# Performance work log

Hardware: AMD Instinct MI355X
Metric: run time of the kernel (lower is better)

## Reference

```python
import jax, jax.numpy as jnp
import numpy as np

# Module hyperparameters (from init_kwargs)
DG = 8          # deformable_groups
KH = KW = 3     # kernel size
STRIDE = 1
PAD = 1
DIL = 1


def conv2d(x, w, b):
    # x: [B,C,H,W], w: [O,I,kh,kw] -> [B,O,Ho,Wo]
    y = jax.lax.conv_general_dilated(
        x, w, window_strides=(STRIDE, STRIDE),
        padding=[(PAD, PAD), (PAD, PAD)],
        rhs_dilation=(DIL, DIL),
        dimension_numbers=('NCHW', 'OIHW', 'NCHW'))
    return y + b[None, :, None, None]


def deform_conv2d(inp, offset, mask, w, b):
    # torchvision.ops.DeformConv2d (v2, with modulation mask), groups=1.
    # offset: [B, 2*DG*K, Ho, Wo] laid out as (dg, k, (dy,dx));
    # mask:   [B, DG*K, Ho, Wo] (already sigmoided).
    B, C, H, W = inp.shape
    Cout = w.shape[0]
    K = KH * KW
    Ho, Wo = offset.shape[2], offset.shape[3]
    Cg = C // DG

    off = offset.reshape(B, DG, K, 2, Ho, Wo)
    # base sampling grid per kernel tap
    ky = jnp.repeat(jnp.arange(KH) * DIL, KW)        # [K]
    kx = jnp.tile(jnp.arange(KW) * DIL, KH)          # [K]
    ybase = jnp.arange(Ho) * STRIDE - PAD            # [Ho]
    xbase = jnp.arange(Wo) * STRIDE - PAD            # [Wo]
    ys = off[:, :, :, 0] + (ky[:, None, None] + ybase[None, :, None])  # [B,DG,K,Ho,Wo]
    xs = off[:, :, :, 1] + (kx[:, None, None] + xbase[None, None, :])

    y0 = jnp.floor(ys)
    x0 = jnp.floor(xs)
    wy = (ys - y0)[:, :, None]   # [B,DG,1,K,Ho,Wo]
    wx = (xs - x0)[:, :, None]
    y0i = y0.astype(jnp.int32)
    x0i = x0.astype(jnp.int32)

    flat = inp.reshape(B, DG, Cg, H * W)

    def gather(yi, xi):
        valid = (yi >= 0) & (yi < H) & (xi >= 0) & (xi < W)        # [B,DG,K,Ho,Wo]
        idx = jnp.clip(yi, 0, H - 1) * W + jnp.clip(xi, 0, W - 1)
        idxf = idx.reshape(B, DG, -1)
        g = jax.vmap(jax.vmap(lambda f, i: jnp.take(f, i, axis=1)))(flat, idxf)
        g = g.reshape(B, DG, Cg, K, Ho, Wo)
        return g * valid[:, :, None].astype(inp.dtype)

    v00 = gather(y0i, x0i)
    v01 = gather(y0i, x0i + 1)
    v10 = gather(y0i + 1, x0i)
    v11 = gather(y0i + 1, x0i + 1)
    val = (v00 * (1 - wy) * (1 - wx) + v01 * (1 - wy) * wx
           + v10 * wy * (1 - wx) + v11 * wy * wx)
    val = val * mask.reshape(B, DG, 1, K, Ho, Wo)
    val = val.reshape(B, C, K, Ho, Wo)
    out = jnp.einsum('bckhw,ock->bohw', val, w.reshape(Cout, C, K))
    return out + b[None, :, None, None]


def setup_inputs() -> dict:
    key = jax.random.key(0)
    ks = jax.random.split(key, 8)
    B, C, Cf, Cout, H, W = 4, 64, 64, 64, 128, 128
    K = KH * KW
    inp = jax.random.normal(ks[0], (B, C, H, W), jnp.float32)
    feature = jax.random.normal(ks[1], (B, Cf, H, W), jnp.float32)
    # conv_offset / conv_mask params (small init so sampled offsets stay local)
    w_off = 0.05 * jax.random.normal(ks[2], (2 * DG * K, Cf, KH, KW), jnp.float32)
    b_off = jnp.zeros((2 * DG * K,), jnp.float32)
    w_mask = 0.05 * jax.random.normal(ks[3], (DG * K, Cf, KH, KW), jnp.float32)
    b_mask = jnp.zeros((DG * K,), jnp.float32)
    # deform conv params
    fan_in = C * KH * KW
    w_dcn = jax.random.normal(ks[4], (Cout, C, KH, KW), jnp.float32) / np.sqrt(fan_in)
    b_dcn = 0.01 * jax.random.normal(ks[5], (Cout,), jnp.float32)
    return {"input": inp, "feature": feature,
            "w_off": w_off, "b_off": b_off,
            "w_mask": w_mask, "b_mask": b_mask,
            "w_dcn": w_dcn, "b_dcn": b_dcn}


def reference(input, feature, w_off, b_off, w_mask, b_mask, w_dcn, b_dcn):
    offset = conv2d(feature, w_off, b_off)
    mask = jax.nn.sigmoid(conv2d(feature, w_mask, b_mask))
    return deform_conv2d(input, offset, mask, w_dcn, b_dcn)
```

## Files before the change

### kernel.cpp

```cpp
#include <hip/hip_runtime.h>
#include <hip/hip_bf16.h>

#define NB 4
#define CIN 64
#define COUT 64
#define HH 128
#define WW 128
#define HW (HH*WW)
#define C_OFF 144
#define C_OM 216
#define C_PAD 224
#define KTOT 576

typedef __attribute__((ext_vector_type(8))) short bf16x8;
typedef __attribute__((ext_vector_type(4))) float f32x4;
typedef __attribute__((ext_vector_type(8))) unsigned short uv8;

__device__ inline unsigned short f2bf(float f) {
    union { float f; unsigned u; } v; v.f = f;
    unsigned r = (v.u + 0x7FFF + ((v.u >> 16) & 1)) >> 16;
    return (unsigned short)r;
}

__device__ inline float bf2f(unsigned short h) {
    union { unsigned u; float f; } v; v.u = ((unsigned)h) << 16; return v.f;
}


__global__ __launch_bounds__(256) void transpose_wdcn(const float* __restrict__ w,
                                                      float* __restrict__ wT) {
    int idx = blockIdx.x * 256 + threadIdx.x;
    if (idx < KTOT * COUT) {
        int o = idx & 63, kk = idx >> 6;
        wT[idx] = w[o * KTOT + kk];
    }
}

__global__ __launch_bounds__(256) void to_nhwc_bf16(const float* __restrict__ f,
                                                    unsigned short* __restrict__ o) {
    int t = blockIdx.x * 256 + threadIdx.x;
    int b = t >> 14, yx = t & 16383;
    const float* src = f + (size_t)b * CIN * HW + yx;
    unsigned short* dst = o + (size_t)t * 64;
#pragma unroll
    for (int c8 = 0; c8 < 8; ++c8) {
        uv8 v;
#pragma unroll
        for (int j = 0; j < 8; ++j) v[j] = f2bf(src[(size_t)(c8 * 8 + j) * HW]);
        *(uv8*)(dst + c8 * 8) = v;
    }
}

__global__ __launch_bounds__(256) void prep_wB(const float* __restrict__ w_off,
                                               const float* __restrict__ w_mask,
                                               unsigned short* __restrict__ wB) {
    int idx = blockIdx.x * 256 + threadIdx.x;
    if (idx >= C_PAD * KTOT) return;
    int co = idx / KTOT, k = idx - co * KTOT;
    int t = k >> 6, ci = k & 63;
    float v = 0.f;
    if (co < C_OFF)      v = w_off[(size_t)co * KTOT + ci * 9 + t];
    else if (co < C_OM)  v = w_mask[(size_t)(co - C_OFF) * KTOT + ci * 9 + t];
    wB[idx] = f2bf(v);
}

__global__ __launch_bounds__(256) void prep_wTf2(const float* __restrict__ w,
                                                 unsigned short* __restrict__ wTf2) {
    int idx = blockIdx.x * 256 + threadIdx.x;
    if (idx >= 72 * 64 * 8) return;
    int q = idx >> 9;
    int co = (idx >> 3) & 63;
    int r = idx & 7;
    int k = q >> 3, dg = q & 7;
    wTf2[idx] = f2bf(w[(size_t)co * KTOT + (dg * 8 + r) * 9 + k]);
}


__global__ __launch_bounds__(256, 4) void dcn_fused(
    const unsigned short* __restrict__ fnhwc,
    const unsigned short* __restrict__ inb,
    const unsigned short* __restrict__ wB,
    const unsigned short* __restrict__ wTf2,
    const float* __restrict__ b_off, const float* __restrict__ b_mask,
    const float* __restrict__ b_dcn,
    float* __restrict__ out)
{
    __shared__ __align__(16) unsigned char smem[72 * 32 * 8 * 2];
    unsigned short* val_q = (unsigned short*)smem;
    unsigned short* Ash   = (unsigned short*)smem;
    unsigned short* Bsh   = (unsigned short*)(smem + 4096);
    float* om_l           = (float*)smem;

    int tid = threadIdx.x;
    int bid = blockIdx.x;
    int b   = bid >> 9;
    int hw0 = (bid & 511) << 5;
    int ho  = hw0 >> 7;
    int wo0 = hw0 & 127;

    int lane = tid & 63, wave = tid >> 6;
    int arow = lane & 15, g = lane >> 4;
    int h  = wave & 1;
    int ws = wave >> 1;

    f32x4 acc[7];
#pragma unroll
    for (int n = 0; n < 7; ++n) acc[n] = (f32x4){0.f, 0.f, 0.f, 0.f};

    int px_w = tid >> 3;
    int c8_w = tid & 7;

    for (int t = 0; t < 9; ++t) {
        int ky = t / 3, kx = t - ky * 3;
        int y = ho + ky - 1;
        bool yv = (unsigned)y < (unsigned)HH;
        __syncthreads();
        {
            int x = wo0 + px_w + kx - 1;
            uv8 v = (uv8){0, 0, 0, 0, 0, 0, 0, 0};
            if (yv && (unsigned)x < (unsigned)WW)
                v = *(const uv8*)(fnhwc + ((size_t)((b * HH + y) * WW + x) << 6) + c8_w * 8);
            int off16 = (c8_w << 4) ^ ((px_w & 7) << 4);
            *(uv8*)((char*)Ash + px_w * 128 + off16) = v;
        }
#pragma unroll
        for (int r = 0; r < 7; ++r) {
            int idx = r * 256 + tid;
            int co = idx >> 3, c8 = idx & 7;
            uv8 v = *(const uv8*)(wB + (size_t)co * KTOT + t * 64 + c8 * 8);
            *(uv8*)((char*)Bsh + co * 128 + ((c8 << 4) ^ ((co & 7) << 4))) = v;
        }
        __syncthreads();
#pragma unroll
        for (int half = 0; half < 2; ++half) {
            int px = h * 16 + arow;
            int kb = half * 64 + g * 16;
            bf16x8 a = *(const bf16x8*)((const char*)Ash + px * 128 + (kb ^ ((px & 7) << 4)));
#pragma unroll
            for (int n = 0; n < 7; ++n) {
                int co = ws * 112 + n * 16 + arow;
                bf16x8 bf = *(const bf16x8*)((const char*)Bsh + co * 128 +
                                             (kb ^ ((co & 7) << 4)));
                acc[n] = __builtin_amdgcn_mfma_f32_16x16x32_bf16(a, bf, acc[n], 0, 0, 0);
            }
        }
    }
    __syncthreads();

#pragma unroll
    for (int n = 0; n < 7; ++n) {
        int co = ws * 112 + n * 16 + arow;
        if (co < C_OM) {
            float bias = (co < C_OFF) ? b_off[co] : b_mask[co - C_OFF];
#pragma unroll
            for (int j = 0; j < 4; ++j) {
                float v = acc[n][j] + bias;
                if (co >= C_OFF) v = 1.f / (1.f + __expf(-v));
                om_l[co * 33 + h * 16 + g * 4 + j] = v;
            }
        }
    }
    __syncthreads();

    int px = tid & 31;
    int dg = tid >> 5;

    float dy[9], dxv[9], mk[9];
#pragma unroll
    for (int k = 0; k < 9; ++k) {
        dy[k]  = om_l[(dg * 18 + 2 * k) * 33 + px];
        dxv[k] = om_l[(dg * 18 + 2 * k + 1) * 33 + px];
        mk[k]  = om_l[(C_OFF + dg * 9 + k) * 33 + px];
    }
    __syncthreads();

    const unsigned short* plane0 = inb + ((size_t)b * HW << 6) + dg * 8;
    float yb = (float)(ho - 1);
    float xb = (float)(wo0 + px - 1);

#pragma unroll
    for (int k = 0; k < 9; ++k) {
        float ys = dy[k] + yb + (float)(k / 3);
        float xs = dxv[k] + xb + (float)(k % 3);
        float y0f = floorf(ys), x0f = floorf(xs);
        float fy = ys - y0f, fx = xs - x0f;
        int y0 = (int)y0f, x0 = (int)x0f;
        bool yv0 = (unsigned)y0 < (unsigned)HH;
        bool yv1 = (unsigned)(y0 + 1) < (unsigned)HH;
        bool xv0 = (unsigned)x0 < (unsigned)WW;
        bool xv1 = (unsigned)(x0 + 1) < (unsigned)WW;
        const unsigned short* pp = plane0 + (y0 * WW + x0) * 64;
        uv8 c00 = (uv8){0,0,0,0,0,0,0,0};
        uv8 c01 = c00, c10 = c00, c11 = c00;
        if (yv0 && xv0) c00 = *(const uv8*)(pp);
        if (yv0 && xv1) c01 = *(const uv8*)(pp + 64);
        if (yv1 && xv0) c10 = *(const uv8*)(pp + 64 * WW);
        if (yv1 && xv1) c11 = *(const uv8*)(pp + 64 * WW + 64);
        uv8 r;
#pragma unroll
        for (int j = 0; j < 8; ++j) {
            float v00 = bf2f(c00[j]), v01 = bf2f(c01[j]);
            float v10 = bf2f(c10[j]), v11 = bf2f(c11[j]);
            float top = v00 + (v01 - v00) * fx;
            float bot = v10 + (v11 - v10) * fx;
            float v = top + (bot - top) * fy;
            r[j] = f2bf(v * mk[k]);
        }
        *(uv8*)(val_q + (k * 8 + dg) * 256 + px * 8) = r;
    }
    __syncthreads();

    int nh = wave >> 1;

    f32x4 dacc[2];
    dacc[0] = dacc[1] = (f32x4){0.f, 0.f, 0.f, 0.f};
#pragma unroll
    for (int s = 0; s < 18; ++s) {
        int q = s * 4 + g;
        bf16x8 a = *(const bf16x8*)(val_q + q * 256 + (h * 16 + arow) * 8);
#pragma unroll
        for (int n = 0; n < 2; ++n) {
            int co = nh * 32 + n * 16 + arow;
            bf16x8 bf = *(const bf16x8*)(wTf2 + ((size_t)q * 64 + co) * 8);
            dacc[n] = __builtin_amdgcn_mfma_f32_16x16x32_bf16(a, bf, dacc[n], 0, 0, 0);
        }
    }

#pragma unroll
    for (int n = 0; n < 2; ++n) {
        int co = nh * 32 + n * 16 + arow;
        float bias = b_dcn[co];
        f32x4 r;
#pragma unroll
        for (int j = 0; j < 4; ++j) r[j] = dacc[n][j] + bias;
        *(f32x4*)(out + (size_t)b * COUT * HW + (size_t)co * HW + hw0 + h * 16 + g * 4) = r;
    }
}


__global__ __launch_bounds__(256) void conv_om_kernel(
    const float* __restrict__ feature,
    const float* __restrict__ w_off, const float* __restrict__ b_off,
    const float* __restrict__ w_mask, const float* __restrict__ b_mask,
    float* __restrict__ om)
{
    int tid = threadIdx.x;
    int p = blockIdx.x * 256 + tid;
    int cg = blockIdx.y;
    int b  = p >> 14;
    int hw = p & (HW - 1);
    int ho = hw >> 7;
    int wo = hw & 127;
    int co0 = cg * 4;

    float acc[4];
    const float* wb[4];
#pragma unroll
    for (int j = 0; j < 4; ++j) {
        int co = co0 + j;
        if (co < C_OFF) { acc[j] = b_off[co];          wb[j] = w_off  + (size_t)co * 576; }
        else            { acc[j] = b_mask[co - C_OFF]; wb[j] = w_mask + (size_t)(co - C_OFF) * 576; }
    }
    const float* fb = feature + (size_t)b * CIN * HW;
    for (int ci = 0; ci < CIN; ++ci) {
        const float* fp = fb + ci * HW;
#pragma unroll
        for (int ky = 0; ky < 3; ++ky) {
            int y = ho + ky - 1;
            bool yvb = (unsigned)y < (unsigned)HH;
#pragma unroll
            for (int kx = 0; kx < 3; ++kx) {
                int x = wo + kx - 1;
                float v = (yvb && (unsigned)x < (unsigned)WW) ? fp[y * WW + x] : 0.f;
                int wi = ci * 9 + ky * 3 + kx;
#pragma unroll
                for (int j = 0; j < 4; ++j) acc[j] += v * wb[j][wi];
            }
        }
    }
    size_t obase = (size_t)b * C_OM * HW + hw;
#pragma unroll
    for (int j = 0; j < 4; ++j) {
        int co = co0 + j;
        float v = acc[j];
        if (co >= C_OFF) v = 1.f / (1.f + __expf(-v));
        om[obase + (size_t)co * HW] = v;
    }
}

__global__ __launch_bounds__(256) void dcn_kernel(
    const float* __restrict__ input,
    const float* __restrict__ om,
    const float* __restrict__ wT,
    const float* __restrict__ b_dcn,
    float* __restrict__ out)
{
    __shared__ float om_l[C_OM * 16];
    __shared__ float val_l[KTOT * 16];

    int tid  = threadIdx.x;
    int tile = blockIdx.x;
    int b    = tile >> 10;
    int hw0  = (tile & 1023) << 4;
    int ho   = hw0 >> 7;
    int wo0  = hw0 & 127;

    const float* omg = om + (size_t)b * C_OM * HW + hw0;
    for (int i = tid; i < C_OM * 16; i += 256) {
        int ch = i >> 4, px = i & 15;
        om_l[i] = omg[(size_t)ch * HW + px];
    }
    __syncthreads();

    for (int pair = tid; pair < 1024; pair += 256) {
        int px = pair & 15, c = pair >> 4;
        int dg = c >> 3;
        const float* plane = input + (size_t)(b * CIN + c) * HW;
        float yb = (float)(ho - 1);
        float xb = (float)(wo0 + px - 1);
#pragma unroll
        for (int k = 0; k < 9; ++k) {
            float dyv = om_l[(dg * 18 + 2 * k) * 16 + px];
            float dxv = om_l[(dg * 18 + 2 * k + 1) * 16 + px];
            float m  = om_l[(C_OFF + dg * 9 + k) * 16 + px];
            float ys = dyv + yb + (float)(k / 3);
            float xs = dxv + xb + (float)(k % 3);
            float y0f = floorf(ys), x0f = floorf(xs);
            float wy = ys - y0f, wx = xs - x0f;
            int y0 = (int)y0f, x0 = (int)x0f;
            bool yv0 = (unsigned)y0 < (unsigned)HH;
            bool yv1 = (unsigned)(y0 + 1) < (unsigned)HH;
            bool xv0 = (unsigned)x0 < (unsigned)WW;
            bool xv1 = (unsigned)(x0 + 1) < (unsigned)WW;
            const float* r0 = plane + y0 * WW + x0;
            float v00 = (yv0 && xv0) ? r0[0]      : 0.f;
            float v01 = (yv0 && xv1) ? r0[1]      : 0.f;
            float v10 = (yv1 && xv0) ? r0[WW]     : 0.f;
            float v11 = (yv1 && xv1) ? r0[WW + 1] : 0.f;
            float top = v00 + (v01 - v00) * wx;
            float bot = v10 + (v11 - v10) * wx;
            float v = top + (bot - top) * wy;
            val_l[(c * 9 + k) * 16 + px] = v * m;
        }
    }
    __syncthreads();

    int o2 = tid & 31;
    int ph = tid >> 5;
    int o0 = o2 * 2, px0 = ph * 2;
    float a00 = b_dcn[o0],     a01 = b_dcn[o0];
    float a10 = b_dcn[o0 + 1], a11 = b_dcn[o0 + 1];
    for (int kk = 0; kk < KTOT; ++kk) {
        float2 wv = *reinterpret_cast<const float2*>(wT + kk * 64 + o0);
        float va = val_l[kk * 16 + px0];
        float vb = val_l[kk * 16 + px0 + 1];
        a00 += wv.x * va; a01 += wv.x * vb;
        a10 += wv.y * va; a11 += wv.y * vb;
    }
    float* ob = out + (size_t)b * COUT * HW + hw0;
    ob[(size_t)o0 * HW + px0]           = a00;
    ob[(size_t)o0 * HW + px0 + 1]       = a01;
    ob[(size_t)(o0 + 1) * HW + px0]     = a10;
    ob[(size_t)(o0 + 1) * HW + px0 + 1] = a11;
}

extern "C" void kernel_launch(void* const* d_in, const int* in_sizes, int n_in,
                              void* d_out, int out_size, void* d_ws, size_t ws_size,
                              hipStream_t stream) {
    const float* input   = (const float*)d_in[0];
    const float* feature = (const float*)d_in[1];
    const float* w_off   = (const float*)d_in[2];
    const float* b_off   = (const float*)d_in[3];
    const float* w_mask  = (const float*)d_in[4];
    const float* b_mask  = (const float*)d_in[5];
    const float* w_dcn   = (const float*)d_in[6];
    const float* b_dcn   = (const float*)d_in[7];
    float* out = (float*)d_out;

    unsigned short* fnhwc = (unsigned short*)d_ws;
    unsigned short* wBp   = fnhwc + (size_t)NB * HW * CIN;
    unsigned short* wTfp  = wBp + (size_t)C_PAD * KTOT;
    unsigned short* inb   = wTfp + 72 * 64 * 8;
    size_t need_full = (size_t)((char*)(inb + (size_t)NB * HW * CIN) - (char*)d_ws);
    size_t need_fb = ((size_t)NB * C_OM * HW + KTOT * COUT) * sizeof(float);

    if (ws_size >= need_full) {
        to_nhwc_bf16<<<NB * HW / 256, 256, 0, stream>>>(feature, fnhwc);
        to_nhwc_bf16<<<NB * HW / 256, 256, 0, stream>>>(input, inb);
        prep_wB<<<(C_PAD * KTOT + 255) / 256, 256, 0, stream>>>(w_off, w_mask, wBp);
        prep_wTf2<<<(72 * 64 * 8 + 255) / 256, 256, 0, stream>>>(w_dcn, wTfp);
        dcn_fused<<<NB * HW / 32, 256, 0, stream>>>(fnhwc, inb, wBp, wTfp,
                                                    b_off, b_mask, b_dcn, out);
    } else if (ws_size >= need_fb) {
        float* om = (float*)d_ws;
        float* wT = om + (size_t)NB * C_OM * HW;
        transpose_wdcn<<<(KTOT * COUT + 255) / 256, 256, 0, stream>>>(w_dcn, wT);
        dim3 cgrid(NB * HW / 256, 54);
        conv_om_kernel<<<cgrid, 256, 0, stream>>>(feature, w_off, b_off, w_mask, b_mask, om);
        dcn_kernel<<<NB * HW / 16, 256, 0, stream>>>(input, om, wT, b_dcn, out);
    }
}
```

Baseline: 94.77 us.

## Process 64 pixels per block to reuse offset-conv weight tiles; merge prep launches

The fused DCN kernel now handles 64 output pixels per block instead of 32. It stages two A tiles per tap and runs two sets of MFMA accumulators, so each weight tile loaded into shared memory serves twice as many pixels. The sampling and output GEMM then run once per 32-pixel half. The two NHWC conversions are merged into one launch, and so are the two weight-prep kernels, to cut launch overhead. The cost is half as many blocks, more accumulator registers (which can lower occupancy under launch_bounds(256,4)), and extra syncs in the per-half epilogue.

```diff
diff --git a/kernel.cpp b/kernel.cpp
--- a/kernel.cpp
+++ b/kernel.cpp
@@ -36,12 +36,17 @@
     }
 }
 
-__global__ __launch_bounds__(256) void to_nhwc_bf16(const float* __restrict__ f,
-                                                    unsigned short* __restrict__ o) {
+__global__ __launch_bounds__(256) void to_nhwc_bf16_2(const float* __restrict__ f0,
+                                                      unsigned short* __restrict__ o0,
+                                                      const float* __restrict__ f1,
+                                                      unsigned short* __restrict__ o1) {
     int t = blockIdx.x * 256 + threadIdx.x;
-    int b = t >> 14, yx = t & 16383;
-    const float* src = f + (size_t)b * CIN * HW + yx;
-    unsigned short* dst = o + (size_t)t * 64;
+    const float* src;
+    unsigned short* dst;
+    int tt = t & 65535;
+    int b = tt >> 14, yx = tt & 16383;
+    if (t < 65536) { src = f0 + (size_t)b * CIN * HW + yx; dst = o0 + (size_t)tt * 64; }
+    else           { src = f1 + (size_t)b * CIN * HW + yx; dst = o1 + (size_t)tt * 64; }
 #pragma unroll
     for (int c8 = 0; c8 < 8; ++c8) {
         uv8 v;
@@ -51,28 +56,27 @@
     }
 }
 
-__global__ __launch_bounds__(256) void prep_wB(const float* __restrict__ w_off,
-                                               const float* __restrict__ w_mask,
-                                               unsigned short* __restrict__ wB) {
+__global__ __launch_bounds__(256) void prep_weights(const float* __restrict__ w_off,
+                                                    const float* __restrict__ w_mask,
+                                                    const float* __restrict__ w_dcn,
+                                                    unsigned short* __restrict__ wB,
+                                                    unsigned short* __restrict__ wTf2) {
     int idx = blockIdx.x * 256 + threadIdx.x;
-    if (idx >= C_PAD * KTOT) return;
-    int co = idx / KTOT, k = idx - co * KTOT;
-    int t = k >> 6, ci = k & 63;
-    float v = 0.f;
-    if (co < C_OFF)      v = w_off[(size_t)co * KTOT + ci * 9 + t];
-    else if (co < C_OM)  v = w_mask[(size_t)(co - C_OFF) * KTOT + ci * 9 + t];
-    wB[idx] = f2bf(v);
-}
-
-__global__ __launch_bounds__(256) void prep_wTf2(const float* __restrict__ w,
-                                                 unsigned short* __restrict__ wTf2) {
-    int idx = blockIdx.x * 256 + threadIdx.x;
-    if (idx >= 72 * 64 * 8) return;
-    int q = idx >> 9;
-    int co = (idx >> 3) & 63;
-    int r = idx & 7;
-    int k = q >> 3, dg = q & 7;
-    wTf2[idx] = f2bf(w[(size_t)co * KTOT + (dg * 8 + r) * 9 + k]);
+    if (idx < C_PAD * KTOT) {
+        int co = idx / KTOT, k = idx - co * KTOT;
+        int t = k >> 6, ci = k & 63;
+        float v = 0.f;
+        if (co < C_OFF)      v = w_off[(size_t)co * KTOT + ci * 9 + t];
+        else if (co < C_OM)  v = w_mask[(size_t)(co - C_OFF) * KTOT + ci * 9 + t];
+        wB[idx] = f2bf(v);
+    } else if (idx < C_PAD * KTOT + 72 * 64 * 8) {
+        int j = idx - C_PAD * KTOT;
+        int q = j >> 9;
+        int co = (j >> 3) & 63;
+        int r = j & 7;
+        int k = q >> 3, dg = q & 7;
+        wTf2[j] = f2bf(w_dcn[(size_t)co * KTOT + (dg * 8 + r) * 9 + k]);
+    }
 }
 
 
@@ -85,16 +89,17 @@
     const float* __restrict__ b_dcn,
     float* __restrict__ out)
 {
-    __shared__ __align__(16) unsigned char smem[72 * 32 * 8 * 2];
+    __shared__ __align__(16) unsigned char smem[36864];
+    unsigned short* Ash0  = (unsigned short*)smem;
+    unsigned short* Ash1  = (unsigned short*)(smem + 4096);
+    unsigned short* Bsh   = (unsigned short*)(smem + 8192);
+    float* om_l           = (float*)smem;
     unsigned short* val_q = (unsigned short*)smem;
-    unsigned short* Ash   = (unsigned short*)smem;
-    unsigned short* Bsh   = (unsigned short*)(smem + 4096);
-    float* om_l           = (float*)smem;
 
     int tid = threadIdx.x;
     int bid = blockIdx.x;
-    int b   = bid >> 9;
-    int hw0 = (bid & 511) << 5;
+    int b   = bid >> 8;
+    int hw0 = (bid & 255) << 6;
     int ho  = hw0 >> 7;
     int wo0 = hw0 & 127;
 
@@ -103,25 +108,31 @@
     int h  = wave & 1;
     int ws = wave >> 1;
 
-    f32x4 acc[7];
-#pragma unroll
-    for (int n = 0; n < 7; ++n) acc[n] = (f32x4){0.f, 0.f, 0.f, 0.f};
+    f32x4 acc0[7], acc1[7];
+#pragma unroll
+    for (int n = 0; n < 7; ++n) {
+        acc0[n] = (f32x4){0.f, 0.f, 0.f, 0.f};
+        acc1[n] = (f32x4){0.f, 0.f, 0.f, 0.f};
+    }
 
     int px_w = tid >> 3;
     int c8_w = tid & 7;
+    const uv8 zero8 = (uv8){0, 0, 0, 0, 0, 0, 0, 0};
 
     for (int t = 0; t < 9; ++t) {
         int ky = t / 3, kx = t - ky * 3;
         int y = ho + ky - 1;
         bool yv = (unsigned)y < (unsigned)HH;
         __syncthreads();
-        {
-            int x = wo0 + px_w + kx - 1;
-            uv8 v = (uv8){0, 0, 0, 0, 0, 0, 0, 0};
+#pragma unroll
+        for (int pt = 0; pt < 2; ++pt) {
+            int x = wo0 + pt * 32 + px_w + kx - 1;
+            uv8 v = zero8;
             if (yv && (unsigned)x < (unsigned)WW)
                 v = *(const uv8*)(fnhwc + ((size_t)((b * HH + y) * WW + x) << 6) + c8_w * 8);
             int off16 = (c8_w << 4) ^ ((px_w & 7) << 4);
-            *(uv8*)((char*)Ash + px_w * 128 + off16) = v;
+            char* dst = (char*)(pt ? Ash1 : Ash0);
+            *(uv8*)(dst + px_w * 128 + off16) = v;
         }
 #pragma unroll
         for (int r = 0; r < 7; ++r) {
@@ -135,105 +146,114 @@
         for (int half = 0; half < 2; ++half) {
             int px = h * 16 + arow;
             int kb = half * 64 + g * 16;
-            bf16x8 a = *(const bf16x8*)((const char*)Ash + px * 128 + (kb ^ ((px & 7) << 4)));
+            bf16x8 a0 = *(const bf16x8*)((const char*)Ash0 + px * 128 + (kb ^ ((px & 7) << 4)));
+            bf16x8 a1 = *(const bf16x8*)((const char*)Ash1 + px * 128 + (kb ^ ((px & 7) << 4)));
 #pragma unroll
             for (int n = 0; n < 7; ++n) {
                 int co = ws * 112 + n * 16 + arow;
                 bf16x8 bf = *(const bf16x8*)((const char*)Bsh + co * 128 +
                                              (kb ^ ((co & 7) << 4)));
-                acc[n] = __builtin_amdgcn_mfma_f32_16x16x32_bf16(a, bf, acc[n], 0, 0, 0);
+                acc0[n] = __builtin_amdgcn_mfma_f32_16x16x32_bf16(a0, bf, acc0[n], 0, 0, 0);
+                acc1[n] = __builtin_amdgcn_mfma_f32_16x16x32_bf16(a1, bf, acc1[n], 0, 0, 0);
             }
         }
     }
     __syncthreads();
 
 #pragma unroll
-    for (int n = 0; n < 7; ++n) {
-        int co = ws * 112 + n * 16 + arow;
-        if (co < C_OM) {
-            float bias = (co < C_OFF) ? b_off[co] : b_mask[co - C_OFF];
-#pragma unroll
-            for (int j = 0; j < 4; ++j) {
-                float v = acc[n][j] + bias;
-                if (co >= C_OFF) v = 1.f / (1.f + __expf(-v));
-                om_l[co * 33 + h * 16 + g * 4 + j] = v;
+    for (int pt = 0; pt < 2; ++pt) {
+        int hw0t = hw0 + pt * 32;
+        int wo0t = wo0 + pt * 32;
+
+#pragma unroll
+        for (int n = 0; n < 7; ++n) {
+            int co = ws * 112 + n * 16 + arow;
+            if (co < C_OM) {
+                float bias = (co < C_OFF) ? b_off[co] : b_mask[co - C_OFF];
+                f32x4 av = pt ? acc1[n] : acc0[n];
+#pragma unroll
+                for (int j = 0; j < 4; ++j) {
+                    float v = av[j] + bias;
+                    if (co >= C_OFF) v = 1.f / (1.f + __expf(-v));
+                    om_l[co * 33 + h * 16 + g * 4 + j] = v;
+                }
             }
         }
-    }
-    __syncthreads();
-
-    int px = tid & 31;
-    int dg = tid >> 5;
-
-    float dy[9], dxv[9], mk[9];
-#pragma unroll
-    for (int k = 0; k < 9; ++k) {
-        dy[k]  = om_l[(dg * 18 + 2 * k) * 33 + px];
-        dxv[k] = om_l[(dg * 18 + 2 * k + 1) * 33 + px];
-        mk[k]  = om_l[(C_OFF + dg * 9 + k) * 33 + px];
-    }
-    __syncthreads();
-
-    const unsigned short* plane0 = inb + ((size_t)b * HW << 6) + dg * 8;
-    float yb = (float)(ho - 1);
-    float xb = (float)(wo0 + px - 1);
-
-#pragma unroll
-    for (int k = 0; k < 9; ++k) {
-        float ys = dy[k] + yb + (float)(k / 3);
-        float xs = dxv[k] + xb + (float)(k % 3);
-        float y0f = floorf(ys), x0f = floorf(xs);
-        float fy = ys - y0f, fx = xs - x0f;
-        int y0 = (int)y0f, x0 = (int)x0f;
-        bool yv0 = (unsigned)y0 < (unsigned)HH;
-        bool yv1 = (unsigned)(y0 + 1) < (unsigned)HH;
-        bool xv0 = (unsigned)x0 < (unsigned)WW;
-        bool xv1 = (unsigned)(x0 + 1) < (unsigned)WW;
-        const unsigned short* pp = plane0 + (y0 * WW + x0) * 64;
-        uv8 c00 = (uv8){0,0,0,0,0,0,0,0};
-        uv8 c01 = c00, c10 = c00, c11 = c00;
-        if (yv0 && xv0) c00 = *(const uv8*)(pp);
-        if (yv0 && xv1) c01 = *(const uv8*)(pp + 64);
-        if (yv1 && xv0) c10 = *(const uv8*)(pp + 64 * WW);
-        if (yv1 && xv1) c11 = *(const uv8*)(pp + 64 * WW + 64);
-        uv8 r;
-#pragma unroll
-        for (int j = 0; j < 8; ++j) {
-            float v00 = bf2f(c00[j]), v01 = bf2f(c01[j]);
-            float v10 = bf2f(c10[j]), v11 = bf2f(c11[j]);
-            float top = v00 + (v01 - v00) * fx;
-            float bot = v10 + (v11 - v10) * fx;
-            float v = top + (bot - top) * fy;
-            r[j] = f2bf(v * mk[k]);
-        }
-        *(uv8*)(val_q + (k * 8 + dg) * 256 + px * 8) = r;
-    }
-    __syncthreads();
-
-    int nh = wave >> 1;
-
-    f32x4 dacc[2];
-    dacc[0] = dacc[1] = (f32x4){0.f, 0.f, 0.f, 0.f};
-#pragma unroll
-    for (int s = 0; s < 18; ++s) {
-        int q = s * 4 + g;
-        bf16x8 a = *(const bf16x8*)(val_q + q * 256 + (h * 16 + arow) * 8);
+        __syncthreads();
+
+        int px = tid & 31;
+        int dg = tid >> 5;
+
+        float dy[9], dxv[9], mk[9];
+#pragma unroll
+        for (int k = 0; k < 9; ++k) {
+            dy[k]  = om_l[(dg * 18 + 2 * k) * 33 + px];
+            dxv[k] = om_l[(dg * 18 + 2 * k + 1) * 33 + px];
+            mk[k]  = om_l[(C_OFF + dg * 9 + k) * 33 + px];
+        }
+        __syncthreads();
+
+        const unsigned short* plane0 = inb + ((size_t)b * HW << 6) + dg * 8;
+        float yb = (float)(ho - 1);
+        float xb = (float)(wo0t + px - 1);
+
+#pragma unroll
+        for (int k = 0; k < 9; ++k) {
+            float ys = dy[k] + yb + (float)(k / 3);
+            float xs = dxv[k] + xb + (float)(k % 3);
+            float y0f = floorf(ys), x0f = floorf(xs);
+            float fy = ys - y0f, fx = xs - x0f;
+            int y0 = (int)y0f, x0 = (int)x0f;
+            bool yv0 = (unsigned)y0 < (unsigned)HH;
+            bool yv1 = (unsigned)(y0 + 1) < (unsigned)HH;
+            bool xv0 = (unsigned)x0 < (unsigned)WW;
+            bool xv1 = (unsigned)(x0 + 1) < (unsigned)WW;
+            const unsigned short* pp = plane0 + (y0 * WW + x0) * 64;
+            uv8 c00 = zero8, c01 = zero8, c10 = zero8, c11 = zero8;
+            if (yv0 && xv0) c00 = *(const uv8*)(pp);
+            if (yv0 && xv1) c01 = *(const uv8*)(pp + 64);
+            if (yv1 && xv0) c10 = *(const uv8*)(pp + 64 * WW);
+            if (yv1 && xv1) c11 = *(const uv8*)(pp + 64 * WW + 64);
+            uv8 r;
+#pragma unroll
+            for (int j = 0; j < 8; ++j) {
+                float v00 = bf2f(c00[j]), v01 = bf2f(c01[j]);
+                float v10 = bf2f(c10[j]), v11 = bf2f(c11[j]);
+                float top = v00 + (v01 - v00) * fx;
+                float bot = v10 + (v11 - v10) * fx;
+                float v = top + (bot - top) * fy;
+                r[j] = f2bf(v * mk[k]);
+            }
+            *(uv8*)(val_q + (k * 8 + dg) * 256 + px * 8) = r;
+        }
+        __syncthreads();
+
+        int nh = wave >> 1;
+
+        f32x4 dacc[2];
+        dacc[0] = dacc[1] = (f32x4){0.f, 0.f, 0.f, 0.f};
+#pragma unroll
+        for (int s = 0; s < 18; ++s) {
+            int q = s * 4 + g;
+            bf16x8 a = *(const bf16x8*)(val_q + q * 256 + (h * 16 + arow) * 8);
+#pragma unroll
+            for (int n = 0; n < 2; ++n) {
+                int co = nh * 32 + n * 16 + arow;
+                bf16x8 bfr = *(const bf16x8*)(wTf2 + ((size_t)q * 64 + co) * 8);
+                dacc[n] = __builtin_amdgcn_mfma_f32_16x16x32_bf16(a, bfr, dacc[n], 0, 0, 0);
+            }
+        }
+
 #pragma unroll
         for (int n = 0; n < 2; ++n) {
             int co = nh * 32 + n * 16 + arow;
-            bf16x8 bf = *(const bf16x8*)(wTf2 + ((size_t)q * 64 + co) * 8);
-            dacc[n] = __builtin_amdgcn_mfma_f32_16x16x32_bf16(a, bf, dacc[n], 0, 0, 0);
-        }
-    }
-
-#pragma unroll
-    for (int n = 0; n < 2; ++n) {
-        int co = nh * 32 + n * 16 + arow;
-        float bias = b_dcn[co];
-        f32x4 r;
-#pragma unroll
-        for (int j = 0; j < 4; ++j) r[j] = dacc[n][j] + bias;
-        *(f32x4*)(out + (size_t)b * COUT * HW + (size_t)co * HW + hw0 + h * 16 + g * 4) = r;
+            float bias = b_dcn[co];
+            f32x4 r;
+#pragma unroll
+            for (int j = 0; j < 4; ++j) r[j] = dacc[n][j] + bias;
+            *(f32x4*)(out + (size_t)b * COUT * HW + (size_t)co * HW + hw0t + h * 16 + g * 4) = r;
+        }
+        __syncthreads();
     }
 }
 
@@ -385,11 +405,10 @@
     size_t need_fb = ((size_t)NB * C_OM * HW + KTOT * COUT) * sizeof(float);
 
     if (ws_size >= need_full) {
-        to_nhwc_bf16<<<NB * HW / 256, 256, 0, stream>>>(feature, fnhwc);
-        to_nhwc_bf16<<<NB * HW / 256, 256, 0, stream>>>(input, inb);
-        prep_wB<<<(C_PAD * KTOT + 255) / 256, 256, 0, stream>>>(w_off, w_mask, wBp);
-        prep_wTf2<<<(72 * 64 * 8 + 255) / 256, 256, 0, stream>>>(w_dcn, wTfp);
-        dcn_fused<<<NB * HW / 32, 256, 0, stream>>>(fnhwc, inb, wBp, wTfp,
+        to_nhwc_bf16_2<<<NB * HW * 2 / 256, 256, 0, stream>>>(feature, fnhwc, input, inb);
+        prep_weights<<<(C_PAD * KTOT + 72 * 64 * 8 + 255) / 256, 256, 0, stream>>>(
+            w_off, w_mask, w_dcn, wBp, wTfp);
+        dcn_fused<<<NB * HW / 64, 256, 0, stream>>>(fnhwc, inb, wBp, wTfp,
                                                     b_off, b_mask, b_dcn, out);
     } else if (ws_size >= need_fb) {
         float* om = (float*)d_ws;
```

Measured after the change: 88.51 us. 6.6% less time.
